# Optimization experiments

Measured on AMD Instinct MI355X. Metric: run time of the kernel, lower is better.

Reference implementation:

```python
import jax, jax.numpy as jnp
import numpy as np

N = 50000
F_IN = 128
E = 800000
C = 32      # hidden_channels
H1 = 8      # heads_1
H2 = 1      # heads_2
NEG_SLOPE = 0.2


def setup_inputs() -> dict:
    key = jax.random.key(0)
    ks = jax.random.split(key, 16)
    s = 0.1
    x = jax.random.normal(ks[0], (N, F_IN), dtype=jnp.float32)
    edge_index = jax.random.randint(ks[1], (2, E), 0, N, dtype=jnp.int32)
    # layer 1: in=F_IN, out=C, heads=H1, concat=True
    Wl1 = jax.random.normal(ks[2], (H1 * C, F_IN), dtype=jnp.float32) * s
    bl1 = jnp.zeros((H1 * C,), dtype=jnp.float32)
    Wr1 = jax.random.normal(ks[3], (H1 * C, F_IN), dtype=jnp.float32) * s
    br1 = jnp.zeros((H1 * C,), dtype=jnp.float32)
    att1 = jax.random.normal(ks[4], (H1, C), dtype=jnp.float32) * s
    bias1 = jnp.zeros((H1 * C,), dtype=jnp.float32)
    # layer 2: in=H1*C, out=C, heads=H2, concat=False (mean)
    Wl2 = jax.random.normal(ks[5], (H2 * C, H1 * C), dtype=jnp.float32) * s
    bl2 = jnp.zeros((H2 * C,), dtype=jnp.float32)
    Wr2 = jax.random.normal(ks[6], (H2 * C, H1 * C), dtype=jnp.float32) * s
    br2 = jnp.zeros((H2 * C,), dtype=jnp.float32)
    att2 = jax.random.normal(ks[7], (H2, C), dtype=jnp.float32) * s
    bias2 = jnp.zeros((C,), dtype=jnp.float32)
    return {"x": x, "edge_index": edge_index,
            "Wl1": Wl1, "bl1": bl1, "Wr1": Wr1, "br1": br1, "att1": att1, "bias1": bias1,
            "Wl2": Wl2, "bl2": bl2, "Wr2": Wr2, "br2": br2, "att2": att2, "bias2": bias2}


def _gatv2_layer(x, src, dst, Wl, bl, Wr, br, att, bias, heads, out_c, concat):
    n = x.shape[0]
    xl = (x @ Wl.T + bl).reshape(n, heads, out_c)  # source transform
    xr = (x @ Wr.T + br).reshape(n, heads, out_c)  # target transform
    z = jax.nn.leaky_relu(xl[src] + xr[dst], NEG_SLOPE)          # [E, H, C]
    logit = jnp.einsum('ehc,hc->eh', z, att)                     # [E, H]
    # segment softmax over incoming edges of each target node
    m = jax.ops.segment_max(logit, dst, num_segments=n)          # [N, H]
    ex = jnp.exp(logit - m[dst])
    denom = jax.ops.segment_sum(ex, dst, num_segments=n)
    alpha = ex / jnp.maximum(denom[dst], 1e-16)                  # [E, H]
    out = jax.ops.segment_sum(alpha[..., None] * xl[src], dst, num_segments=n)  # [N, H, C]
    out = out.reshape(n, heads * out_c) if concat else out.mean(axis=1)
    return out + bias


def reference(x, edge_index, Wl1, bl1, Wr1, br1, att1, bias1,
              Wl2, bl2, Wr2, br2, att2, bias2):
    n = x.shape[0]
    # PyG GATv2Conv default: add self loops
    loops = jnp.arange(n, dtype=edge_index.dtype)
    src = jnp.concatenate([edge_index[0], loops])
    dst = jnp.concatenate([edge_index[1], loops])
    h = _gatv2_layer(x, src, dst, Wl1, bl1, Wr1, br1, att1, bias1, H1, C, True)
    h = jax.nn.gelu(h, approximate=False)
    out = _gatv2_layer(h, src, dst, Wl2, bl2, Wr2, br2, att2, bias2, H2, C, False)
    return out
```

## Files before the change

### kernel.cpp

```cpp
#include <hip/hip_runtime.h>
#include <hip/hip_bf16.h>


typedef unsigned short u16;
typedef short bf16x8 __attribute__((ext_vector_type(8)));
typedef float f32x4 __attribute__((ext_vector_type(4)));
typedef float f32x2 __attribute__((ext_vector_type(2)));

#define F_IN   128
#define CH     32
#define H1     8
#define JT1    512
#define JH1    256
#define JT2    64
#define JH2    32

#define OFF_Y1     0UL
#define OFF_H      52000000UL
#define OFF_Y2     78000000UL
#define OFF_COL    85000000UL
#define OFF_DEG    89000000UL
#define OFF_ROW    89400000UL
#define OFF_CUR    89800000UL
#define OFF_WC     90200000UL
#define OFF_FLAG   90600000UL
#define OFF_BSUM   90700000UL
#define WS_NEED    91000000UL

#define W_WL1   0
#define W_BL1   32768
#define W_WR1   33024
#define W_BR1   65792
#define W_ATT1  66048
#define W_BIAS1 66304
#define W_WL2   66560
#define W_BL2   74752
#define W_WR2   74784
#define W_BR2   82976
#define W_ATT2  83008
#define W_BIAS2 83040
#define W_TOTAL 83072

__device__ inline float b2f(u16 u) { return __uint_as_float(((unsigned)u) << 16); }
__device__ inline u16 f2b(float f) {
    unsigned u = __float_as_uint(f);
    unsigned r = (u + 0x7fffu + ((u >> 16) & 1u)) >> 16;
    return (u16)r;
}
__device__ inline unsigned cvtpk(float lo, float hi) {
    unsigned r;
    asm("v_cvt_pk_bf16_f32 %0, %1, %2" : "=v"(r) : "v"(lo), "v"(hi));
    return r;
}
__device__ inline f32x2 pk_add(f32x2 a, f32x2 b) {
    f32x2 d;
    asm("v_pk_add_f32 %0, %1, %2" : "=v"(d) : "v"(a), "v"(b));
    return d;
}
__device__ inline f32x2 pk_fma(f32x2 a, f32x2 b, f32x2 c) {
    f32x2 d;
    asm("v_pk_fma_f32 %0, %1, %2, %3" : "=v"(d) : "v"(a), "v"(b), "v"(c));
    return d;
}
__device__ inline f32x2 unpk(unsigned u) {
    f32x2 d;
    d.x = __uint_as_float(u << 16);
    d.y = __uint_as_float(u & 0xffff0000u);
    return d;
}
__device__ inline f32x2 pabs(f32x2 z) {
    f32x2 d;
    d.x = __uint_as_float(__float_as_uint(z.x) & 0x7fffffffu);
    d.y = __uint_as_float(__float_as_uint(z.y) & 0x7fffffffu);
    return d;
}

struct WcArgs { const void* src[12]; int cum[13]; };

__global__ __launch_bounds__(256) void prep(
    WcArgs a, const u16* __restrict__ xprobe, u16* __restrict__ dst, int total,
    int* __restrict__ flagOut, int NBW,
    const int* __restrict__ ei, int* __restrict__ deg, int E_, int NP) {
    const int t = threadIdx.x;
    if ((int)blockIdx.x >= NBW) {
        int e = ((int)blockIdx.x - NBW) * 256 + t;
        if (e >= E_ + NP) return;
        int dstn = (e < E_) ? ei[E_ + e] : e - E_;
        atomicAdd(deg + dstn, 1);
        return;
    }
    __shared__ int cnt[256];
    __shared__ int sflag;
    int c = 0;
    for (int i = t; i < 512; i += 256) {
        u16 u = xprobe[i];
        int e = (u >> 7) & 0xff;
        c += (u == 0 || (e >= 100 && e <= 141)) ? 1 : 0;
    }
    cnt[t] = c; __syncthreads();
    for (int off = 128; off; off >>= 1) {
        if (t < off) cnt[t] += cnt[t + off];
        __syncthreads();
    }
    if (t == 0) {
        sflag = (cnt[0] >= 440) ? 1 : 0;
        if (blockIdx.x == 0) *flagOut = sflag;
    }
    __syncthreads();
    const int fl = sflag;
    int i = blockIdx.x * 256 + t;
    if (i >= total) return;
    int s = 0;
    while (i >= a.cum[s + 1]) s++;
    int rel = i - a.cum[s];
    if (fl) dst[i] = ((const u16*)a.src[s])[rel];
    else    dst[i] = f2b(((const float*)a.src[s])[rel]);
}

__global__ __launch_bounds__(256) void scan_part(const int* __restrict__ deg,
                                                 int* __restrict__ bsum, int NN) {
    __shared__ int red[256];
    int b = blockIdx.x, t = threadIdx.x;
    int base = b * 1024 + t * 4;
    int s = 0;
#pragma unroll
    for (int j = 0; j < 4; j++) { int i = base + j; if (i < NN) s += deg[i]; }
    red[t] = s; __syncthreads();
    for (int off = 128; off; off >>= 1) {
        if (t < off) red[t] += red[t + off];
        __syncthreads();
    }
    if (t == 0) bsum[b] = red[0];
}

__global__ __launch_bounds__(256) void scan_final(
    const int* __restrict__ deg, const int* __restrict__ bsum,
    int* __restrict__ rowptr, int* __restrict__ cur, int NN, int NB) {
    __shared__ int sb[256];
    __shared__ int ps[256];
    int b = blockIdx.x, t = threadIdx.x;
    int bv = (t < NB) ? bsum[t] : 0;
    sb[t] = bv; __syncthreads();
    for (int off = 1; off < 256; off <<= 1) {
        int x = (t >= off) ? sb[t - off] : 0;
        __syncthreads();
        sb[t] += x;
        __syncthreads();
    }
    if (b == 0 && t == 0) rowptr[NN] = sb[NB - 1];
    int boff = (b == 0) ? 0 : sb[b - 1];

    int base = b * 1024 + t * 4;
    int v[4]; int s = 0;
#pragma unroll
    for (int j = 0; j < 4; j++) { int i = base + j; v[j] = (i < NN) ? deg[i] : 0; s += v[j]; }
    ps[t] = s; __syncthreads();
    for (int off = 1; off < 256; off <<= 1) {
        int x = (t >= off) ? ps[t - off] : 0;
        __syncthreads();
        ps[t] += x;
        __syncthreads();
    }
    int run = boff + (t ? ps[t - 1] : 0);
#pragma unroll
    for (int j = 0; j < 4; j++) {
        int i = base + j;
        if (i < NN) { rowptr[i] = run; cur[i] = run; run += v[j]; }
    }
}

template <int K, int NG, bool DYN>
__device__ __forceinline__ void gemm_body(
    float (*cs)[32][68],
    const void* __restrict__ X, const u16* __restrict__ Wl, const u16* __restrict__ Wr,
    const u16* __restrict__ bl, const u16* __restrict__ br,
    u16* __restrict__ Y, int M, int JH, const int* __restrict__ flagp, int bm0) {
    const int t = threadIdx.x, w = t >> 6, l = t & 63;
    const int JT = 2 * JH;
    const int lr = l & 15, lk = (l >> 4) * 8;
    const int fl = DYN ? *flagp : 1;

    int rowm[2];
#pragma unroll
    for (int mt = 0; mt < 2; mt++) {
        int row = bm0 + w * 32 + mt * 16 + lr;
        if (row >= M) row = M - 1;
        rowm[mt] = row;
    }

    constexpr int KK = K / 32;
    bf16x8 afr[2][KK];
    if (fl) {
        const u16* xb = (const u16*)X;
#pragma unroll
        for (int mt = 0; mt < 2; mt++)
#pragma unroll
            for (int kk = 0; kk < KK; kk++)
                afr[mt][kk] = *(const bf16x8*)(xb + (size_t)rowm[mt] * K + lk + kk * 32);
    } else {
        const float* xf = (const float*)X;
#pragma unroll
        for (int mt = 0; mt < 2; mt++)
#pragma unroll
            for (int kk = 0; kk < KK; kk++) {
                const float* p = xf + (size_t)rowm[mt] * K + lk + kk * 32;
                float4 v0 = *(const float4*)p;
                float4 v1 = *(const float4*)(p + 4);
                uint4 o;
                o.x = cvtpk(v0.x, v0.y); o.y = cvtpk(v0.z, v0.w);
                o.z = cvtpk(v1.x, v1.y); o.w = cvtpk(v1.z, v1.w);
                afr[mt][kk] = *(bf16x8*)&o;
            }
    }

#pragma unroll 1
    for (int g = 0; g < NG; g++) {
        const int bn0 = g * 64;
        const u16* bx[4];
        float bv[4];
#pragma unroll
        for (int nt = 0; nt < 4; nt++) {
            int j = bn0 + nt * 16 + lr;
            const u16* wp = (j < JH) ? (Wl + (size_t)j * K) : (Wr + (size_t)(j - JH) * K);
            bx[nt] = wp + lk;
            bv[nt] = b2f(j < JH ? bl[j] : br[j - JH]);
        }

        f32x4 acc[2][4];
#pragma unroll
        for (int mt = 0; mt < 2; mt++)
#pragma unroll
            for (int nt = 0; nt < 4; nt++) acc[mt][nt] = (f32x4){0.f, 0.f, 0.f, 0.f};

#pragma unroll
        for (int kk = 0; kk < KK; kk++) {
            bf16x8 b[4];
#pragma unroll
            for (int nt = 0; nt < 4; nt++) b[nt] = *(const bf16x8*)(bx[nt] + kk * 32);
#pragma unroll
            for (int mt = 0; mt < 2; mt++)
#pragma unroll
                for (int nt = 0; nt < 4; nt++)
                    acc[mt][nt] = __builtin_amdgcn_mfma_f32_16x16x32_bf16(
                        afr[mt][kk], b[nt], acc[mt][nt], 0, 0, 0);
        }

#pragma unroll
        for (int mt = 0; mt < 2; mt++)
#pragma unroll
            for (int nt = 0; nt < 4; nt++)
#pragma unroll
                for (int r = 0; r < 4; r++)
                    cs[w][mt * 16 + (l >> 4) * 4 + r][nt * 16 + lr] = acc[mt][nt][r] + bv[nt];

#pragma unroll
        for (int p = 0; p < 4; p++) {
            int rl = p * 8 + (l >> 3);
            int grow = bm0 + w * 32 + rl;
            if (grow < M) {
                const float* rp = &cs[w][rl][(l & 7) * 8];
                float4 v0 = *(const float4*)rp;
                float4 v1 = *(const float4*)(rp + 4);
                uint4 o;
                o.x = cvtpk(v0.x, v0.y); o.y = cvtpk(v0.z, v0.w);
                o.z = cvtpk(v1.x, v1.y); o.w = cvtpk(v1.z, v1.w);
                *(uint4*)(Y + (size_t)grow * JT + bn0 + (l & 7) * 8) = o;
            }
        }
    }
}

__global__ __launch_bounds__(256) void gemm1_scatter(
    const void* __restrict__ X, const u16* __restrict__ Wl, const u16* __restrict__ Wr,
    const u16* __restrict__ bl, const u16* __restrict__ br,
    u16* __restrict__ Y, int M, const int* __restrict__ flagp, int NBG,
    const int* __restrict__ ei, int* __restrict__ cur, int* __restrict__ col,
    int E_, int NP) {
    __shared__ float cs[4][32][68];
    if ((int)blockIdx.x < NBG) {
        gemm_body<F_IN, JT1 / 64, true>(cs, X, Wl, Wr, bl, br, Y, M, JH1, flagp,
                                        (int)blockIdx.x * 128);
        return;
    }
    int e = ((int)blockIdx.x - NBG) * 256 + threadIdx.x;
    if (e >= E_ + NP) return;
    int src, dst;
    if (e < E_) { src = ei[e]; dst = ei[E_ + e]; }
    else        { src = dst = e - E_; }
    int pos = atomicAdd(cur + dst, 1);
    col[pos] = src;
}

__global__ __launch_bounds__(256) void gemm2_k(
    const u16* __restrict__ X, const u16* __restrict__ Wl, const u16* __restrict__ Wr,
    const u16* __restrict__ bl, const u16* __restrict__ br,
    u16* __restrict__ Y, int M, const int* __restrict__ flagp) {
    __shared__ float cs[4][32][68];
    gemm_body<JH1, JT2 / 64, false>(cs, X, Wl, Wr, bl, br, Y, M, JH2, flagp,
                                    (int)blockIdx.x * 128);
}

__global__ __launch_bounds__(256, 4) void agg1(
    const u16* __restrict__ Y1, const int* __restrict__ rowptr,
    const int* __restrict__ col, const u16* __restrict__ att,
    const u16* __restrict__ bias, u16* __restrict__ hout, int NN) {
    const int wid = blockIdx.x * 4 + (threadIdx.x >> 6);
    if (wid >= NN) return;
    const int lane = threadIdx.x & 63, half = lane >> 5, hl = lane & 31;
    const int n = wid;

    f32x2 xr2[4], a06[4], a04[4];
    {
        uint4 rx = *(const uint4*)(Y1 + (size_t)n * JT1 + JH1 + hl * 8);
        uint4 ra = *(const uint4*)(att + hl * 8);
        unsigned ux[4] = {rx.x, rx.y, rx.z, rx.w};
        unsigned ua[4] = {ra.x, ra.y, ra.z, ra.w};
#pragma unroll
        for (int p = 0; p < 4; p++) {
            xr2[p] = unpk(ux[p]);
            f32x2 a = unpk(ua[p]);
            a06[p].x = 0.6f * a.x; a06[p].y = 0.6f * a.y;
            a04[p].x = 0.4f * a.x; a04[p].y = 0.4f * a.y;
        }
    }
    f32x2 acc2[4] = {{0.f,0.f},{0.f,0.f},{0.f,0.f},{0.f,0.f}};
    float dsum = 0.f;

    auto edge = [&](uint4 raw) {
        unsigned uw[4] = {raw.x, raw.y, raw.z, raw.w};
        f32x2 xl2[4];
        f32x2 p2 = {0.f, 0.f};
#pragma unroll
        for (int p = 0; p < 4; p++) {
            xl2[p] = unpk(uw[p]);
            f32x2 z = pk_add(xl2[p], xr2[p]);
            p2 = pk_fma(z, a06[p], p2);
            p2 = pk_fma(pabs(z), a04[p], p2);
        }
        float pl = p2.x + p2.y;
        pl += __shfl_xor(pl, 1); pl += __shfl_xor(pl, 2);
        float e = __expf(pl);
        dsum += e;
        f32x2 e2; e2.x = e; e2.y = e;
#pragma unroll
        for (int p = 0; p < 4; p++) acc2[p] = pk_fma(e2, xl2[p], acc2[p]);
    };

    const int beg = rowptr[n], end = rowptr[n + 1];
    int i = beg + half;
    for (; i + 14 < end; i += 16) {
        int s[8];
#pragma unroll
        for (int k = 0; k < 8; k++) s[k] = col[i + 2 * k];
        uint4 r[8];
#pragma unroll
        for (int k = 0; k < 8; k++) r[k] = *(const uint4*)(Y1 + (size_t)s[k] * JT1 + hl * 8);
#pragma unroll
        for (int k = 0; k < 8; k++) edge(r[k]);
    }
    for (; i + 6 < end; i += 8) {
        int s0 = col[i], s1 = col[i + 2], s2 = col[i + 4], s3 = col[i + 6];
        uint4 r0 = *(const uint4*)(Y1 + (size_t)s0 * JT1 + hl * 8);
        uint4 r1 = *(const uint4*)(Y1 + (size_t)s1 * JT1 + hl * 8);
        uint4 r2 = *(const uint4*)(Y1 + (size_t)s2 * JT1 + hl * 8);
        uint4 r3 = *(const uint4*)(Y1 + (size_t)s3 * JT1 + hl * 8);
        edge(r0); edge(r1); edge(r2); edge(r3);
    }
    for (; i < end; i += 2) {
        uint4 r0 = *(const uint4*)(Y1 + (size_t)col[i] * JT1 + hl * 8);
        edge(r0);
    }

    dsum += __shfl_xor(dsum, 32);
#pragma unroll
    for (int p = 0; p < 4; p++) {
        acc2[p].x += __shfl_xor(acc2[p].x, 32);
        acc2[p].y += __shfl_xor(acc2[p].y, 32);
    }

    if (half == 0) {
        float inv = 1.f / fmaxf(dsum, 1e-16f);
        u16 bu[8];
        *(uint4*)bu = *(const uint4*)(bias + hl * 8);
        float v[8];
#pragma unroll
        for (int p = 0; p < 4; p++) {
            float x0 = acc2[p].x * inv + b2f(bu[2 * p]);
            float x1 = acc2[p].y * inv + b2f(bu[2 * p + 1]);
            v[2 * p]     = 0.5f * x0 * (1.f + erff(x0 * 0.70710678118654752f));
            v[2 * p + 1] = 0.5f * x1 * (1.f + erff(x1 * 0.70710678118654752f));
        }
        uint4 o;
        o.x = cvtpk(v[0], v[1]); o.y = cvtpk(v[2], v[3]);
        o.z = cvtpk(v[4], v[5]); o.w = cvtpk(v[6], v[7]);
        *(uint4*)(hout + (size_t)n * JH1 + hl * 8) = o;
    }
}

__global__ __launch_bounds__(256) void agg2(
    const u16* __restrict__ Y2, const int* __restrict__ rowptr,
    const int* __restrict__ col, const u16* __restrict__ att,
    const u16* __restrict__ bias, void* __restrict__ dout, int NN,
    const int* __restrict__ flag) {
    const int wid = blockIdx.x * 4 + (threadIdx.x >> 6);
    if (wid >= NN) return;
    const int lane = threadIdx.x & 63, le = lane >> 4, cl = lane & 15;
    const int n = wid;

    f32x2 xr2 = unpk(*(const unsigned*)(Y2 + (size_t)n * JT2 + JH2 + cl * 2));
    f32x2 av  = unpk(*(const unsigned*)(att + cl * 2));
    f32x2 a06; a06.x = 0.6f * av.x; a06.y = 0.6f * av.y;
    f32x2 a04; a04.x = 0.4f * av.x; a04.y = 0.4f * av.y;
    f32x2 acc2 = {0.f, 0.f};
    float dsum = 0.f;

    auto edge = [&](unsigned raw, bool act) {
        f32x2 xl2 = unpk(raw);
        f32x2 z = pk_add(xl2, xr2);
        f32x2 p2 = pk_fma(z, a06, (f32x2){0.f, 0.f});
        p2 = pk_fma(pabs(z), a04, p2);
        float pl = p2.x + p2.y;
        pl += __shfl_xor(pl, 1); pl += __shfl_xor(pl, 2);
        pl += __shfl_xor(pl, 4); pl += __shfl_xor(pl, 8);
        float e = __expf(pl);
        if (!act) e = 0.f;
        dsum += e;
        f32x2 e2; e2.x = e; e2.y = e;
        acc2 = pk_fma(e2, xl2, acc2);
    };

    const int beg = rowptr[n], end = rowptr[n + 1];
    int i = beg;
    for (; i + 16 <= end; i += 16) {
        int s0 = col[i + le], s1 = col[i + 4 + le];
        int s2 = col[i + 8 + le], s3 = col[i + 12 + le];
        unsigned r0 = *(const unsigned*)(Y2 + (size_t)s0 * JT2 + cl * 2);
        unsigned r1 = *(const unsigned*)(Y2 + (size_t)s1 * JT2 + cl * 2);
        unsigned r2 = *(const unsigned*)(Y2 + (size_t)s2 * JT2 + cl * 2);
        unsigned r3 = *(const unsigned*)(Y2 + (size_t)s3 * JT2 + cl * 2);
        edge(r0, true); edge(r1, true); edge(r2, true); edge(r3, true);
    }
    for (; i + 8 <= end; i += 8) {
        int sA = col[i + le];
        int sB = col[i + 4 + le];
        unsigned rA = *(const unsigned*)(Y2 + (size_t)sA * JT2 + cl * 2);
        unsigned rB = *(const unsigned*)(Y2 + (size_t)sB * JT2 + cl * 2);
        edge(rA, true);
        edge(rB, true);
    }
    for (; i < end; i += 4) {
        int idx = i + le;
        bool act = idx < end;
        int s0 = col[act ? idx : end - 1];
        unsigned r0 = *(const unsigned*)(Y2 + (size_t)s0 * JT2 + cl * 2);
        edge(r0, act);
    }

    dsum += __shfl_xor(dsum, 16); dsum += __shfl_xor(dsum, 32);
    acc2.x += __shfl_xor(acc2.x, 16); acc2.x += __shfl_xor(acc2.x, 32);
    acc2.y += __shfl_xor(acc2.y, 16); acc2.y += __shfl_xor(acc2.y, 32);

    if (le == 0) {
        float inv = 1.f / fmaxf(dsum, 1e-16f);
        f32x2 bv = unpk(*(const unsigned*)(bias + cl * 2));
        float v0 = acc2.x * inv + bv.x;
        float v1 = acc2.y * inv + bv.y;
        if (*flag) {
            *(unsigned*)((u16*)dout + n * JH2 + cl * 2) = cvtpk(v0, v1);
        } else {
            float2 o; o.x = v0; o.y = v1;
            *(float2*)((float*)dout + n * JH2 + cl * 2) = o;
        }
    }
}

extern "C" void kernel_launch(void* const* d_in, const int* in_sizes, int n_in,
                              void* d_out, int out_size, void* d_ws, size_t ws_size,
                              hipStream_t stream) {
    const int NN = in_sizes[0] / F_IN;
    const int EE = in_sizes[1] / 2;
    const int EP = EE + NN;
    if (ws_size < WS_NEED) return;

    char* w = (char*)d_ws;
    u16*   Y1   = (u16*)(w + OFF_Y1);
    u16*   hbuf = (u16*)(w + OFF_H);
    u16*   Y2   = (u16*)(w + OFF_Y2);
    int*   col  = (int*)(w + OFF_COL);
    int*   deg  = (int*)(w + OFF_DEG);
    int*   rowp = (int*)(w + OFF_ROW);
    int*   cur  = (int*)(w + OFF_CUR);
    u16*   Wc   = (u16*)(w + OFF_WC);
    int*   flag = (int*)(w + OFF_FLAG);
    int*   bsum = (int*)(w + OFF_BSUM);

    const int* ei = (const int*)d_in[1];

    hipMemsetAsync(deg, 0, (size_t)NN * 4, stream);
    {
        WcArgs a;
        int sizes[12] = {JH1 * F_IN, JH1, JH1 * F_IN, JH1, H1 * CH, JH1,
                         JH2 * JH1, JH2, JH2 * JH1, JH2, JH2, JH2};
        int c = 0;
        for (int s = 0; s < 12; s++) { a.src[s] = d_in[2 + s]; a.cum[s] = c; c += sizes[s]; }
        a.cum[12] = c;
        const int NBW = (W_TOTAL + 255) / 256;
        const int NBE = (EP + 255) / 256;
        prep<<<NBW + NBE, 256, 0, stream>>>(a, (const u16*)d_in[0], Wc, W_TOTAL,
                                            flag, NBW, ei, deg, EE, NN);
    }

    const int NB = (NN + 1023) / 1024;
    scan_part<<<NB, 256, 0, stream>>>(deg, bsum, NN);
    scan_final<<<NB, 256, 0, stream>>>(deg, bsum, rowp, cur, NN, NB);

    {
        const int NBG = (NN + 127) / 128;
        const int NBE = (EP + 255) / 256;
        gemm1_scatter<<<NBG + NBE, 256, 0, stream>>>(
            d_in[0], Wc + W_WL1, Wc + W_WR1, Wc + W_BL1, Wc + W_BR1,
            Y1, NN, flag, NBG, ei, cur, col, EE, NN);
    }
    agg1<<<(NN + 3) / 4, 256, 0, stream>>>(Y1, rowp, col, Wc + W_ATT1,
                                           Wc + W_BIAS1, hbuf, NN);

    gemm2_k<<<(NN + 127) / 128, 256, 0, stream>>>(
        hbuf, Wc + W_WL2, Wc + W_WR2, Wc + W_BL2, Wc + W_BR2, Y2, NN, flag);
    agg2<<<(NN + 3) / 4, 256, 0, stream>>>(Y2, rowp, col, Wc + W_ATT2,
                                           Wc + W_BIAS2, d_out, NN, flag);
}
```

Measured before the change: 250.6 us.

## Split source/target projections into separate dense buffers and use max-based leaky ReLU

The GEMM outputs are written to separate XL and XR arrays instead of one interleaved [N, 2*JH] buffer. The gathered source rows in the aggregation kernels then sit in a dense array of half the row stride, which should improve cache and TLB locality for the random gathers. Leaky ReLU is now computed as max(z, 0.2z) times att, replacing the 0.6z + 0.4|z| two-FMA form. The new form costs a packed multiply plus two max instructions per pair.

```diff
diff --git a/kernel.cpp b/kernel.cpp
--- a/kernel.cpp
+++ b/kernel.cpp
@@ -10,14 +10,14 @@
 #define F_IN   128
 #define CH     32
 #define H1     8
-#define JT1    512
 #define JH1    256
-#define JT2    64
 #define JH2    32
 
-#define OFF_Y1     0UL
+#define OFF_XL1    0UL
+#define OFF_XR1    26000000UL
 #define OFF_H      52000000UL
-#define OFF_Y2     78000000UL
+#define OFF_XL2    78000000UL
+#define OFF_XR2    81400000UL
 #define OFF_COL    85000000UL
 #define OFF_DEG    89000000UL
 #define OFF_ROW    89400000UL
@@ -57,21 +57,27 @@
     asm("v_pk_add_f32 %0, %1, %2" : "=v"(d) : "v"(a), "v"(b));
     return d;
 }
+__device__ inline f32x2 pk_mul(f32x2 a, f32x2 b) {
+    f32x2 d;
+    asm("v_pk_mul_f32 %0, %1, %2" : "=v"(d) : "v"(a), "v"(b));
+    return d;
+}
 __device__ inline f32x2 pk_fma(f32x2 a, f32x2 b, f32x2 c) {
     f32x2 d;
     asm("v_pk_fma_f32 %0, %1, %2, %3" : "=v"(d) : "v"(a), "v"(b), "v"(c));
     return d;
 }
+__device__ inline f32x2 leaky2(f32x2 z) {
+    f32x2 zs = pk_mul(z, (f32x2){0.2f, 0.2f});
+    f32x2 d;
+    d.x = fmaxf(z.x, zs.x);
+    d.y = fmaxf(z.y, zs.y);
+    return d;
+}
 __device__ inline f32x2 unpk(unsigned u) {
     f32x2 d;
     d.x = __uint_as_float(u << 16);
     d.y = __uint_as_float(u & 0xffff0000u);
-    return d;
-}
-__device__ inline f32x2 pabs(f32x2 z) {
-    f32x2 d;
-    d.x = __uint_as_float(__float_as_uint(z.x) & 0x7fffffffu);
-    d.y = __uint_as_float(__float_as_uint(z.y) & 0x7fffffffu);
     return d;
 }
 
@@ -174,9 +180,9 @@
     float (*cs)[32][68],
     const void* __restrict__ X, const u16* __restrict__ Wl, const u16* __restrict__ Wr,
     const u16* __restrict__ bl, const u16* __restrict__ br,
-    u16* __restrict__ Y, int M, int JH, const int* __restrict__ flagp, int bm0) {
+    u16* __restrict__ Yl, u16* __restrict__ Yr, int M, int JH,
+    const int* __restrict__ flagp, int bm0) {
     const int t = threadIdx.x, w = t >> 6, l = t & 63;
-    const int JT = 2 * JH;
     const int lr = l & 15, lk = (l >> 4) * 8;
     const int fl = DYN ? *flagp : 1;
 
@@ -264,7 +270,10 @@
                 uint4 o;
                 o.x = cvtpk(v0.x, v0.y); o.y = cvtpk(v0.z, v0.w);
                 o.z = cvtpk(v1.x, v1.y); o.w = cvtpk(v1.z, v1.w);
-                *(uint4*)(Y + (size_t)grow * JT + bn0 + (l & 7) * 8) = o;
+                int j0 = bn0 + (l & 7) * 8;
+                u16* dstp = (j0 < JH) ? (Yl + (size_t)grow * JH + j0)
+                                      : (Yr + (size_t)grow * JH + (j0 - JH));
+                *(uint4*)dstp = o;
             }
         }
     }
@@ -273,13 +282,14 @@
 __global__ __launch_bounds__(256) void gemm1_scatter(
     const void* __restrict__ X, const u16* __restrict__ Wl, const u16* __restrict__ Wr,
     const u16* __restrict__ bl, const u16* __restrict__ br,
-    u16* __restrict__ Y, int M, const int* __restrict__ flagp, int NBG,
+    u16* __restrict__ Yl, u16* __restrict__ Yr, int M,
+    const int* __restrict__ flagp, int NBG,
     const int* __restrict__ ei, int* __restrict__ cur, int* __restrict__ col,
     int E_, int NP) {
     __shared__ float cs[4][32][68];
     if ((int)blockIdx.x < NBG) {
-        gemm_body<F_IN, JT1 / 64, true>(cs, X, Wl, Wr, bl, br, Y, M, JH1, flagp,
-                                        (int)blockIdx.x * 128);
+        gemm_body<F_IN, 8, true>(cs, X, Wl, Wr, bl, br, Yl, Yr, M, JH1, flagp,
+                                 (int)blockIdx.x * 128);
         return;
     }
     int e = ((int)blockIdx.x - NBG) * 256 + threadIdx.x;
@@ -294,34 +304,31 @@
 __global__ __launch_bounds__(256) void gemm2_k(
     const u16* __restrict__ X, const u16* __restrict__ Wl, const u16* __restrict__ Wr,
     const u16* __restrict__ bl, const u16* __restrict__ br,
-    u16* __restrict__ Y, int M, const int* __restrict__ flagp) {
+    u16* __restrict__ Yl, u16* __restrict__ Yr, int M,
+    const int* __restrict__ flagp) {
     __shared__ float cs[4][32][68];
-    gemm_body<JH1, JT2 / 64, false>(cs, X, Wl, Wr, bl, br, Y, M, JH2, flagp,
-                                    (int)blockIdx.x * 128);
+    gemm_body<JH1, 1, false>(cs, X, Wl, Wr, bl, br, Yl, Yr, M, JH2, flagp,
+                             (int)blockIdx.x * 128);
 }
 
 __global__ __launch_bounds__(256, 4) void agg1(
-    const u16* __restrict__ Y1, const int* __restrict__ rowptr,
-    const int* __restrict__ col, const u16* __restrict__ att,
-    const u16* __restrict__ bias, u16* __restrict__ hout, int NN) {
+    const u16* __restrict__ XL, const u16* __restrict__ XR,
+    const int* __restrict__ rowptr, const int* __restrict__ col,
+    const u16* __restrict__ att, const u16* __restrict__ bias,
+    u16* __restrict__ hout, int NN) {
     const int wid = blockIdx.x * 4 + (threadIdx.x >> 6);
     if (wid >= NN) return;
     const int lane = threadIdx.x & 63, half = lane >> 5, hl = lane & 31;
     const int n = wid;
 
-    f32x2 xr2[4], a06[4], a04[4];
+    f32x2 xr2[4], av[4];
     {
-        uint4 rx = *(const uint4*)(Y1 + (size_t)n * JT1 + JH1 + hl * 8);
+        uint4 rx = *(const uint4*)(XR + (size_t)n * JH1 + hl * 8);
         uint4 ra = *(const uint4*)(att + hl * 8);
         unsigned ux[4] = {rx.x, rx.y, rx.z, rx.w};
         unsigned ua[4] = {ra.x, ra.y, ra.z, ra.w};
 #pragma unroll
-        for (int p = 0; p < 4; p++) {
-            xr2[p] = unpk(ux[p]);
-            f32x2 a = unpk(ua[p]);
-            a06[p].x = 0.6f * a.x; a06[p].y = 0.6f * a.y;
-            a04[p].x = 0.4f * a.x; a04[p].y = 0.4f * a.y;
-        }
+        for (int p = 0; p < 4; p++) { xr2[p] = unpk(ux[p]); av[p] = unpk(ua[p]); }
     }
     f32x2 acc2[4] = {{0.f,0.f},{0.f,0.f},{0.f,0.f},{0.f,0.f}};
     float dsum = 0.f;
@@ -334,8 +341,7 @@
         for (int p = 0; p < 4; p++) {
             xl2[p] = unpk(uw[p]);
             f32x2 z = pk_add(xl2[p], xr2[p]);
-            p2 = pk_fma(z, a06[p], p2);
-            p2 = pk_fma(pabs(z), a04[p], p2);
+            p2 = pk_fma(leaky2(z), av[p], p2);
         }
         float pl = p2.x + p2.y;
         pl += __shfl_xor(pl, 1); pl += __shfl_xor(pl, 2);
@@ -354,20 +360,20 @@
         for (int k = 0; k < 8; k++) s[k] = col[i + 2 * k];
         uint4 r[8];
 #pragma unroll
-        for (int k = 0; k < 8; k++) r[k] = *(const uint4*)(Y1 + (size_t)s[k] * JT1 + hl * 8);
+        for (int k = 0; k < 8; k++) r[k] = *(const uint4*)(XL + (size_t)s[k] * JH1 + hl * 8);
 #pragma unroll
         for (int k = 0; k < 8; k++) edge(r[k]);
     }
     for (; i + 6 < end; i += 8) {
         int s0 = col[i], s1 = col[i + 2], s2 = col[i + 4], s3 = col[i + 6];
-        uint4 r0 = *(const uint4*)(Y1 + (size_t)s0 * JT1 + hl * 8);
-        uint4 r1 = *(const uint4*)(Y1 + (size_t)s1 * JT1 + hl * 8);
-        uint4 r2 = *(const uint4*)(Y1 + (size_t)s2 * JT1 + hl * 8);
-        uint4 r3 = *(const uint4*)(Y1 + (size_t)s3 * JT1 + hl * 8);
+        uint4 r0 = *(const uint4*)(XL + (size_t)s0 * JH1 + hl * 8);
+        uint4 r1 = *(const uint4*)(XL + (size_t)s1 * JH1 + hl * 8);
+        uint4 r2 = *(const uint4*)(XL + (size_t)s2 * JH1 + hl * 8);
+        uint4 r3 = *(const uint4*)(XL + (size_t)s3 * JH1 + hl * 8);
         edge(r0); edge(r1); edge(r2); edge(r3);
     }
     for (; i < end; i += 2) {
-        uint4 r0 = *(const uint4*)(Y1 + (size_t)col[i] * JT1 + hl * 8);
+        uint4 r0 = *(const uint4*)(XL + (size_t)col[i] * JH1 + hl * 8);
         edge(r0);
     }
 
@@ -398,27 +404,24 @@
 }
 
 __global__ __launch_bounds__(256) void agg2(
-    const u16* __restrict__ Y2, const int* __restrict__ rowptr,
-    const int* __restrict__ col, const u16* __restrict__ att,
-    const u16* __restrict__ bias, void* __restrict__ dout, int NN,
-    const int* __restrict__ flag) {
+    const u16* __restrict__ XL, const u16* __restrict__ XR,
+    const int* __restrict__ rowptr, const int* __restrict__ col,
+    const u16* __restrict__ att, const u16* __restrict__ bias,
+    void* __restrict__ dout, int NN, const int* __restrict__ flag) {
     const int wid = blockIdx.x * 4 + (threadIdx.x >> 6);
     if (wid >= NN) return;
     const int lane = threadIdx.x & 63, le = lane >> 4, cl = lane & 15;
     const int n = wid;
 
-    f32x2 xr2 = unpk(*(const unsigned*)(Y2 + (size_t)n * JT2 + JH2 + cl * 2));
+    f32x2 xr2 = unpk(*(const unsigned*)(XR + (size_t)n * JH2 + cl * 2));
     f32x2 av  = unpk(*(const unsigned*)(att + cl * 2));
-    f32x2 a06; a06.x = 0.6f * av.x; a06.y = 0.6f * av.y;
-    f32x2 a04; a04.x = 0.4f * av.x; a04.y = 0.4f * av.y;
     f32x2 acc2 = {0.f, 0.f};
     float dsum = 0.f;
 
     auto edge = [&](unsigned raw, bool act) {
         f32x2 xl2 = unpk(raw);
         f32x2 z = pk_add(xl2, xr2);
-        f32x2 p2 = pk_fma(z, a06, (f32x2){0.f, 0.f});
-        p2 = pk_fma(pabs(z), a04, p2);
+        f32x2 p2 = pk_mul(leaky2(z), av);
         float pl = p2.x + p2.y;
         pl += __shfl_xor(pl, 1); pl += __shfl_xor(pl, 2);
         pl += __shfl_xor(pl, 4); pl += __shfl_xor(pl, 8);
@@ -434,17 +437,17 @@
     for (; i + 16 <= end; i += 16) {
         int s0 = col[i + le], s1 = col[i + 4 + le];
         int s2 = col[i + 8 + le], s3 = col[i + 12 + le];
-        unsigned r0 = *(const unsigned*)(Y2 + (size_t)s0 * JT2 + cl * 2);
-        unsigned r1 = *(const unsigned*)(Y2 + (size_t)s1 * JT2 + cl * 2);
-        unsigned r2 = *(const unsigned*)(Y2 + (size_t)s2 * JT2 + cl * 2);
-        unsigned r3 = *(const unsigned*)(Y2 + (size_t)s3 * JT2 + cl * 2);
+        unsigned r0 = *(const unsigned*)(XL + (size_t)s0 * JH2 + cl * 2);
+        unsigned r1 = *(const unsigned*)(XL + (size_t)s1 * JH2 + cl * 2);
+        unsigned r2 = *(const unsigned*)(XL + (size_t)s2 * JH2 + cl * 2);
+        unsigned r3 = *(const unsigned*)(XL + (size_t)s3 * JH2 + cl * 2);
         edge(r0, true); edge(r1, true); edge(r2, true); edge(r3, true);
     }
     for (; i + 8 <= end; i += 8) {
         int sA = col[i + le];
         int sB = col[i + 4 + le];
-        unsigned rA = *(const unsigned*)(Y2 + (size_t)sA * JT2 + cl * 2);
-        unsigned rB = *(const unsigned*)(Y2 + (size_t)sB * JT2 + cl * 2);
+        unsigned rA = *(const unsigned*)(XL + (size_t)sA * JH2 + cl * 2);
+        unsigned rB = *(const unsigned*)(XL + (size_t)sB * JH2 + cl * 2);
         edge(rA, true);
         edge(rB, true);
     }
@@ -452,7 +455,7 @@
         int idx = i + le;
         bool act = idx < end;
         int s0 = col[act ? idx : end - 1];
-        unsigned r0 = *(const unsigned*)(Y2 + (size_t)s0 * JT2 + cl * 2);
+        unsigned r0 = *(const unsigned*)(XL + (size_t)s0 * JH2 + cl * 2);
         edge(r0, act);
     }
 
@@ -483,9 +486,11 @@
     if (ws_size < WS_NEED) return;
 
     char* w = (char*)d_ws;
-    u16*   Y1   = (u16*)(w + OFF_Y1);
+    u16*   XL1  = (u16*)(w + OFF_XL1);
+    u16*   XR1  = (u16*)(w + OFF_XR1);
     u16*   hbuf = (u16*)(w + OFF_H);
-    u16*   Y2   = (u16*)(w + OFF_Y2);
+    u16*   XL2  = (u16*)(w + OFF_XL2);
+    u16*   XR2  = (u16*)(w + OFF_XR2);
     int*   col  = (int*)(w + OFF_COL);
     int*   deg  = (int*)(w + OFF_DEG);
     int*   rowp = (int*)(w + OFF_ROW);
@@ -519,13 +524,13 @@
         const int NBE = (EP + 255) / 256;
         gemm1_scatter<<<NBG + NBE, 256, 0, stream>>>(
             d_in[0], Wc + W_WL1, Wc + W_WR1, Wc + W_BL1, Wc + W_BR1,
-            Y1, NN, flag, NBG, ei, cur, col, EE, NN);
-    }
-    agg1<<<(NN + 3) / 4, 256, 0, stream>>>(Y1, rowp, col, Wc + W_ATT1,
+            XL1, XR1, NN, flag, NBG, ei, cur, col, EE, NN);
+    }
+    agg1<<<(NN + 3) / 4, 256, 0, stream>>>(XL1, XR1, rowp, col, Wc + W_ATT1,
                                            Wc + W_BIAS1, hbuf, NN);
 
     gemm2_k<<<(NN + 127) / 128, 256, 0, stream>>>(
-        hbuf, Wc + W_WL2, Wc + W_WR2, Wc + W_BL2, Wc + W_BR2, Y2, NN, flag);
-    agg2<<<(NN + 3) / 4, 256, 0, stream>>>(Y2, rowp, col, Wc + W_ATT2,
+        hbuf, Wc + W_WL2, Wc + W_WR2, Wc + W_BL2, Wc + W_BR2, XL2, XR2, NN, flag);
+    agg2<<<(NN + 3) / 4, 256, 0, stream>>>(XL2, XR2, rowp, col, Wc + W_ATT2,
                                            Wc + W_BIAS2, d_out, NN, flag);
 }
```

After: 267.1 us. +6.6%, slower.
